# Optimization experiments

Measured on AMD Instinct MI355X. Metric: run time of the kernel, lower is better.

Reference implementation:

```python
import jax, jax.numpy as jnp
import numpy as np

BETA = 0.9      # LIF leak factor
THR = 1.0       # firing threshold
SLOPE = 5.0     # surrogate-gradient sigmoid slope


def spike_fn(v):
    # Heaviside forward, sigmoid surrogate gradient (straight-through).
    hard = (v > THR).astype(v.dtype)
    surr = jax.nn.sigmoid(SLOPE * (v - THR))
    return hard + (surr - jax.lax.stop_gradient(surr))


def setup_inputs() -> dict:
    key = jax.random.key(0)
    ks = jax.random.split(key, 4)
    B, T, IN, H, OUT = 16, 128, 1024, 4096, 1024
    def lin_w(k, out_d, in_d):
        bound = 1.0 / np.sqrt(in_d)
        return jax.random.uniform(k, (out_d, in_d), jnp.float32, -bound, bound)
    return {
        "x": jax.random.normal(ks[0], (B, T, IN), jnp.float32),
        "w1": lin_w(ks[1], H, IN), "b1": jnp.zeros((H,), jnp.float32),
        "w2": lin_w(ks[2], H, H),  "b2": jnp.zeros((H,), jnp.float32),
        "w3": lin_w(ks[3], OUT, H), "b3": jnp.zeros((OUT,), jnp.float32),
    }


def reference(x, w1, b1, w2, b2, w3, b3):
    # x: [B, T, IN]; sequential per-timestep SNN feed-forward, readout = sum over time.
    B = x.shape[0]
    H = w1.shape[0]
    v0 = jnp.zeros((B, H), x.dtype)

    def step(carry, xt):                      # xt: [B, IN]
        v1, v2 = carry
        h1 = xt @ w1.T + b1                   # [B, H]
        v1 = BETA * v1 + h1
        s1 = spike_fn(v1)
        v1 = v1 - s1 * THR                    # soft reset
        h2 = s1 @ w2.T + b2                   # [B, H]
        v2 = BETA * v2 + h2
        s2 = spike_fn(v2)
        v2 = v2 - s2 * THR
        logits = s2 @ w3.T + b3               # [B, OUT]
        return (v1, v2), logits

    _, logits = jax.lax.scan(step, (v0, v0), jnp.swapaxes(x, 0, 1))  # [T, B, OUT]
    return logits.sum(axis=0)                 # readout_mode == 'sum'
```

## Files before the change

### kernel.cpp

```cpp
#include <hip/hip_runtime.h>
#include <hip/hip_bf16.h>

#define B_   16
#define T_   128
#define IN_  1024
#define H_   4096
#define OUT_ 1024
#define M_   (B_ * T_)

typedef __attribute__((ext_vector_type(8))) short short8;
typedef __attribute__((ext_vector_type(4))) float f32x4;
typedef __attribute__((ext_vector_type(4))) int i32x4;
typedef __attribute__((ext_vector_type(4))) unsigned short u16x4;
typedef unsigned short u16;
typedef signed char i8;

__device__ inline u16 f2bf_rne(float f) {
  unsigned u = __float_as_uint(f);
  unsigned r = u + 0x7FFFu + ((u >> 16) & 1u);
  return (u16)(r >> 16);
}
__device__ inline float bf2f(u16 s) {
  return __uint_as_float(((unsigned)s) << 16);
}
__device__ inline int pack4(int a, int b, int c, int d) {
  return (a & 255) | ((b & 255) << 8) | ((c & 255) << 16) | ((d & 255) << 24);
}

__device__ inline void xcd_swizzle(int bid0, int& bnI, int& bmI) {
  const int xcd = bid0 & 7;
  const int loc = bid0 >> 3;
  bnI = (xcd & 3) * 8 + (loc & 7);
  bmI = (xcd >> 2) * 8 + (loc >> 3);
}

#define NX_  (M_ * IN_)
#define NW1_ (H_ * IN_)
#define NW2_ (H_ * H_)

__device__ inline void split4bf(const float4 f, u16* __restrict__ hi,
                                u16* __restrict__ lo, size_t e) {
  u16x4 h, l;
  h.x = f2bf_rne(f.x); l.x = f2bf_rne(f.x - bf2f(h.x));
  h.y = f2bf_rne(f.y); l.y = f2bf_rne(f.y - bf2f(h.y));
  h.z = f2bf_rne(f.z); l.z = f2bf_rne(f.z - bf2f(h.z));
  h.w = f2bf_rne(f.w); l.w = f2bf_rne(f.w - bf2f(h.w));
  *(u16x4*)(hi + e) = h;
  *(u16x4*)(lo + e) = l;
}

__device__ inline void splitw2_1(float w, int& c0, int& c1, int& c2) {
  int wf = __float2int_rn(w * 268435456.0f);
  c0 = (wf + 32768) >> 16;
  int r0 = wf - (c0 << 16);
  if (r0 >= 32640) { c0 += 1; r0 -= 65536; }
  c1 = (r0 + 128) >> 8;
  c2 = r0 - (c1 << 8);
}

__global__ void split_xw1_kernel(const float4* __restrict__ x,
                                 const float4* __restrict__ w1,
                                 u16* __restrict__ xh, u16* __restrict__ xl,
                                 u16* __restrict__ w1h, u16* __restrict__ w1l) {
  const int total4 = (NX_ + NW1_) / 4;
  for (int i = blockIdx.x * blockDim.x + threadIdx.x; i < total4;
       i += gridDim.x * blockDim.x) {
    if (i < NX_ / 4) {
      split4bf(x[i], xh, xl, (size_t)i * 4);
    } else {
      int j = i - NX_ / 4;
      split4bf(w1[j], w1h, w1l, (size_t)j * 4);
    }
  }
}

#define BK1 64

__global__ __launch_bounds__(256, 2) void gemm1_rec(
    const u16* __restrict__ Ah, const u16* __restrict__ Al,
    const u16* __restrict__ Bh, const u16* __restrict__ Bl,
    const float* __restrict__ bias, i8* __restrict__ s1out,
    const float4* __restrict__ w2src,
    i8* __restrict__ p0, i8* __restrict__ p1, i8* __restrict__ p2) {
  __shared__ __align__(16) char smem[65536];
  u16* sAh = (u16*)smem;
  u16* sAl = (u16*)(smem + 16384);
  u16* sBh = (u16*)(smem + 32768);
  u16* sBl = (u16*)(smem + 49152);

  const int tid  = threadIdx.x;
  const int lane = tid & 63;
  const int wid  = tid >> 6;
  const int wm   = (wid >> 1) * 64;
  const int wn   = (wid & 1) * 64;
  const int bid  = blockIdx.y * 32 + blockIdx.x;
  int bnI, bmI;
  xcd_swizzle(bid, bnI, bmI);
  const int bm = bmI * 128;
  const int bn = bnI * 128;

  const int sdst = (tid & 7) * 8;
  const int scol = (((tid & 7) ^ ((tid >> 3) & 7)) * 8);
  const int q8   = (lane >> 4) * 8;
  const int rsw  = (lane & 7) * 8;

  f32x4 acc[4][4];
#pragma unroll
  for (int i = 0; i < 4; ++i)
#pragma unroll
    for (int j = 0; j < 4; ++j) acc[i][j] = (f32x4){0.f, 0.f, 0.f, 0.f};

  const int wbase = bid * 8192 + tid * 2;
  float4 wfa = w2src[wbase];
  float4 wfb = w2src[wbase + 1];

#pragma unroll 1
  for (int it = 0; it < IN_ / BK1; ++it) {
    const int kt = it * BK1;
    __syncthreads();
#pragma unroll
    for (int l = 0; l < 4; ++l) {
      int row = l * 32 + (tid >> 3);
      size_t ga = (size_t)(bm + row) * IN_ + kt + scol;
      size_t gb = (size_t)(bn + row) * IN_ + kt + scol;
      int ld = row * BK1 + sdst;
      __builtin_amdgcn_global_load_lds(
          (const __attribute__((address_space(1))) unsigned int*)(Ah + ga),
          (__attribute__((address_space(3))) unsigned int*)(&sAh[ld]), 16, 0, 0);
      __builtin_amdgcn_global_load_lds(
          (const __attribute__((address_space(1))) unsigned int*)(Al + ga),
          (__attribute__((address_space(3))) unsigned int*)(&sAl[ld]), 16, 0, 0);
      __builtin_amdgcn_global_load_lds(
          (const __attribute__((address_space(1))) unsigned int*)(Bh + gb),
          (__attribute__((address_space(3))) unsigned int*)(&sBh[ld]), 16, 0, 0);
      __builtin_amdgcn_global_load_lds(
          (const __attribute__((address_space(1))) unsigned int*)(Bl + gb),
          (__attribute__((address_space(3))) unsigned int*)(&sBl[ld]), 16, 0, 0);
    }
    __syncthreads();

    const int nit = (it + 1 < 16) ? it + 1 : 15;
    float4 nfa = w2src[wbase + nit * 512];
    float4 nfb = w2src[wbase + nit * 512 + 1];

    {
      const int sbase = bid * 8192 + it * 512 + tid * 2;
#pragma unroll
      for (int u = 0; u < 2; ++u) {
        float4 f = u ? wfb : wfa;
        int a0, a1, a2, b0, b1, b2, c0, c1, c2, d0, d1, d2;
        splitw2_1(f.x, a0, a1, a2);
        splitw2_1(f.y, b0, b1, b2);
        splitw2_1(f.z, c0, c1, c2);
        splitw2_1(f.w, d0, d1, d2);
        size_t e = (size_t)(sbase + u) * 4;
        *(int*)(p0 + e) = pack4(a0, b0, c0, d0);
        *(int*)(p1 + e) = pack4(a1, b1, c1, d1);
        *(int*)(p2 + e) = pack4(a2, b2, c2, d2);
      }
    }

#pragma unroll
    for (int ks = 0; ks < BK1; ks += 32) {
      const int swz = (ks + q8) ^ rsw;
      short8 ah[4], al[4], bh[4], bl[4];
#pragma unroll
      for (int i = 0; i < 4; ++i) {
        int ro = (wm + i * 16 + (lane & 15)) * BK1 + swz;
        ah[i] = *(const short8*)&sAh[ro];
        al[i] = *(const short8*)&sAl[ro];
      }
#pragma unroll
      for (int j = 0; j < 4; ++j) {
        int ro = (wn + j * 16 + (lane & 15)) * BK1 + swz;
        bh[j] = *(const short8*)&sBh[ro];
        bl[j] = *(const short8*)&sBl[ro];
      }
#pragma unroll
      for (int i = 0; i < 4; ++i)
#pragma unroll
        for (int j = 0; j < 4; ++j) {
          acc[i][j] = __builtin_amdgcn_mfma_f32_16x16x32_bf16(ah[i], bh[j], acc[i][j], 0, 0, 0);
          acc[i][j] = __builtin_amdgcn_mfma_f32_16x16x32_bf16(ah[i], bl[j], acc[i][j], 0, 0, 0);
          acc[i][j] = __builtin_amdgcn_mfma_f32_16x16x32_bf16(al[i], bh[j], acc[i][j], 0, 0, 0);
          acc[i][j] = __builtin_amdgcn_mfma_f32_16x16x32_bf16(al[i], bl[j], acc[i][j], 0, 0, 0);
        }
    }

    wfa = nfa;
    wfb = nfb;
  }

  float* hl = (float*)smem;
  const int c = tid & 127;
  const float bv = bias[bn + c];
  float v = 0.0f;
  __syncthreads();
#pragma unroll
  for (int half = 0; half < 2; ++half) {
    if (wm == half * 64) {
#pragma unroll
      for (int i = 0; i < 4; ++i)
#pragma unroll
        for (int j = 0; j < 4; ++j) {
          int col = wn + j * 16 + (lane & 15);
#pragma unroll
          for (int r = 0; r < 4; ++r) {
            int lrow = i * 16 + (lane >> 4) * 4 + r;
            hl[lrow * 128 + col] = acc[i][j][r];
          }
        }
    }
    __syncthreads();
    if (tid < 128) {
      for (int tt = 0; tt < 64; ++tt) {
        float h = hl[tt * 128 + c] + bv;
        v = 0.9f * v + h;
        i8 sp = 0;
        if (v > 1.0f) { sp = 1; v -= 1.0f; }
        s1out[(size_t)(bm + half * 64 + tt) * H_ + bn + c] = sp;
      }
    }
    __syncthreads();
  }
}

#define G2_OFFP1 16384
#define G2_OFFP2 24576
#define G2_OFFP0 32768
#define G2_BUFS  40960

#define G2_GLD(srcp, ldsp)                                                  \
  __builtin_amdgcn_global_load_lds(                                         \
      (const __attribute__((address_space(1))) unsigned int*)(srcp),        \
      (__attribute__((address_space(3))) unsigned int*)(ldsp), 16, 0, 0)

__global__ __launch_bounds__(512, 2) void gemm2_i8(
    const i8* __restrict__ A,
    const i8* __restrict__ P0, const i8* __restrict__ P1,
    const i8* __restrict__ P2,
    const float* __restrict__ bias, float* __restrict__ s2out) {
  __shared__ __align__(16) char smem[81920];

  const int tid  = threadIdx.x;
  const int lane = tid & 63;
  const int wid  = tid >> 6;
  const int wm   = (wid >> 1) * 64;
  const int wn   = (wid & 1) * 64;

  const int bid = blockIdx.x;
  const int xcd = bid & 7, loc = bid >> 3;
  const int bmI = (xcd & 3) * 2 + (loc & 1);
  const int bnI = (xcd >> 2) * 16 + (loc >> 1);
  const int bm = bmI * 256, bn = bnI * 128;

  const int j8   = tid & 7;
  const int r8   = tid >> 3;
  const int cc   = j8 ^ (r8 & 7);
  const int srow = 2 * r8 + (cc >> 2);
  const int scol = (cc & 3) * 16;
  const int dst0 = r8 * 128 + j8 * 16;
  const size_t gA = (size_t)(bm + srow) * H_ + scol;
  const size_t gP = (size_t)(bn + srow) * H_ + scol;

  const int r15 = lane & 15, qk = lane >> 4;
  const int lro = (r15 >> 1) * 128 +
                  (((((r15 & 1) << 2) + qk) ^ ((r15 >> 1) & 7)) * 16);
  const int abase = wm * 64 + lro;
  const int bbase = wn * 64 + lro;

  i32x4 acc0[4][4], acc1[4][4], acc2[4][4];
#pragma unroll
  for (int i = 0; i < 4; ++i)
#pragma unroll
    for (int j = 0; j < 4; ++j) {
      acc0[i][j] = (i32x4){0, 0, 0, 0};
      acc1[i][j] = (i32x4){0, 0, 0, 0};
      acc2[i][j] = (i32x4){0, 0, 0, 0};
    }

  G2_GLD(A + gA, smem + dst0);
  G2_GLD(A + gA + (size_t)128 * H_, smem + 8192 + dst0);
  G2_GLD(P1 + gP, smem + G2_OFFP1 + dst0);
  G2_GLD(P2 + gP, smem + G2_OFFP2 + dst0);
  G2_GLD(P0 + gP, smem + G2_OFFP0 + dst0);
  G2_GLD(A + gA + 64, smem + G2_BUFS + dst0);
  G2_GLD(A + gA + (size_t)128 * H_ + 64, smem + G2_BUFS + 8192 + dst0);
  G2_GLD(P1 + gP + 64, smem + G2_BUFS + G2_OFFP1 + dst0);
  asm volatile("s_waitcnt vmcnt(5)" ::: "memory");
  __builtin_amdgcn_s_barrier();

#pragma unroll 1
  for (int t = 0; t < 64; ++t) {
    char* cur = smem + (t & 1) * G2_BUFS;
    char* nxt = smem + ((t + 1) & 1) * G2_BUFS;
    const int kt1 = (t < 63 ? t + 1 : 63) << 6;
    const int kt2 = (t < 62 ? t + 2 : 63) << 6;

    i32x4 a[4], b[4];

#pragma unroll
    for (int i = 0; i < 4; ++i)
      a[i] = *(const i32x4*)(cur + abase + i * 1024);
#pragma unroll
    for (int j = 0; j < 4; ++j)
      b[j] = *(const i32x4*)(cur + G2_OFFP1 + bbase + j * 1024);
    G2_GLD(P2 + gP + kt1, nxt + G2_OFFP2 + dst0);
    G2_GLD(P0 + gP + kt1, nxt + G2_OFFP0 + dst0);
    __builtin_amdgcn_s_barrier();
    asm volatile("s_waitcnt lgkmcnt(0)" ::: "memory");
    __builtin_amdgcn_s_setprio(1);
#pragma unroll
    for (int i = 0; i < 4; ++i)
#pragma unroll
      for (int j = 0; j < 4; ++j)
        acc1[i][j] = __builtin_amdgcn_mfma_i32_16x16x64_i8(a[i], b[j], acc1[i][j], 0, 0, 0);
    __builtin_amdgcn_s_setprio(0);
    asm volatile("s_waitcnt vmcnt(5)" ::: "memory");
    __builtin_amdgcn_s_barrier();

#pragma unroll
    for (int j = 0; j < 4; ++j)
      b[j] = *(const i32x4*)(cur + G2_OFFP2 + bbase + j * 1024);
    G2_GLD(A + gA + kt2, cur + dst0);
    G2_GLD(A + gA + (size_t)128 * H_ + kt2, cur + 8192 + dst0);
    G2_GLD(P1 + gP + kt2, cur + G2_OFFP1 + dst0);
    __builtin_amdgcn_s_barrier();
    asm volatile("s_waitcnt lgkmcnt(0)" ::: "memory");
    __builtin_amdgcn_s_setprio(1);
#pragma unroll
    for (int i = 0; i < 4; ++i)
#pragma unroll
      for (int j = 0; j < 4; ++j)
        acc2[i][j] = __builtin_amdgcn_mfma_i32_16x16x64_i8(a[i], b[j], acc2[i][j], 0, 0, 0);
    __builtin_amdgcn_s_setprio(0);
    __builtin_amdgcn_s_barrier();

#pragma unroll
    for (int j = 0; j < 4; ++j)
      b[j] = *(const i32x4*)(cur + G2_OFFP0 + bbase + j * 1024);
    __builtin_amdgcn_s_barrier();
    asm volatile("s_waitcnt lgkmcnt(0)" ::: "memory");
    __builtin_amdgcn_s_setprio(1);
#pragma unroll
    for (int i = 0; i < 4; ++i)
#pragma unroll
      for (int j = 0; j < 4; ++j)
        acc0[i][j] = __builtin_amdgcn_mfma_i32_16x16x64_i8(a[i], b[j], acc0[i][j], 0, 0, 0);
    __builtin_amdgcn_s_setprio(0);
    asm volatile("s_waitcnt vmcnt(5)" ::: "memory");
    __builtin_amdgcn_s_barrier();
  }

  float* hl = (float*)smem;
  const int ec = tid & 127;
  const float bv = bias[bn + ec];
  asm volatile("s_waitcnt vmcnt(0)" ::: "memory");
  __syncthreads();
#pragma unroll
  for (int hb = 0; hb < 2; ++hb) {
    float v = 0.0f, cnt = 0.0f;
#pragma unroll
    for (int half = 0; half < 2; ++half) {
      const int hq = hb * 2 + half;
      if (wm == hq * 64) {
#pragma unroll
        for (int i = 0; i < 4; ++i)
#pragma unroll
          for (int j = 0; j < 4; ++j) {
            int col = wn + j * 16 + (lane & 15);
#pragma unroll
            for (int r = 0; r < 4; ++r) {
              int lrow = i * 16 + (lane >> 4) * 4 + r;
              float val = 0x1p-28f * (float)((acc1[i][j][r] << 8) + acc2[i][j][r]) +
                          0x1p-12f * (float)acc0[i][j][r];
              hl[lrow * 128 + col] = val;
            }
          }
      }
      __syncthreads();
      if (tid < 128) {
        for (int tt = 0; tt < 64; ++tt) {
          float h = hl[tt * 128 + ec] + bv;
          v = 0.9f * v + h;
          if (v > 1.0f) { cnt += 1.0f; v -= 1.0f; }
        }
      }
      __syncthreads();
    }
    if (tid < 128) s2out[(size_t)(2 * bmI + hb) * H_ + bn + ec] = cnt;
  }
}

__global__ void out_gemm_kernel(const float* __restrict__ s2sum,
                                const float* __restrict__ w3,
                                const float* __restrict__ b3,
                                float* __restrict__ out) {
  int o = blockIdx.x;
  int lane = threadIdx.x;
  float acc[B_];
#pragma unroll
  for (int b = 0; b < B_; ++b) acc[b] = 0.f;
  const float* wrow = w3 + (size_t)o * H_;
  for (int i = 0; i < H_ / 64; ++i) {
    float w = wrow[i * 64 + lane];
#pragma unroll
    for (int b = 0; b < B_; ++b)
      acc[b] += w * s2sum[b * H_ + i * 64 + lane];
  }
#pragma unroll
  for (int b = 0; b < B_; ++b) {
    float v = acc[b];
#pragma unroll
    for (int off = 32; off > 0; off >>= 1) v += __shfl_xor(v, off);
    if (lane == b) out[b * OUT_ + o] = v + (float)T_ * b3[o];
  }
}

extern "C" void kernel_launch(void* const* d_in, const int* in_sizes, int n_in,
                              void* d_out, int out_size, void* d_ws, size_t ws_size,
                              hipStream_t stream) {
  const float* x  = (const float*)d_in[0];
  const float* w1 = (const float*)d_in[1];
  const float* b1 = (const float*)d_in[2];
  const float* w2 = (const float*)d_in[3];
  const float* b2 = (const float*)d_in[4];
  const float* w3 = (const float*)d_in[5];
  const float* b3 = (const float*)d_in[6];
  float* out = (float*)d_out;

  char* ws = (char*)d_ws;
  i8*    s1    = (i8*)(ws);
  u16*   x_hi  = (u16*)(ws + 8388608);
  u16*   x_lo  = (u16*)(ws + 12582912);
  u16*   w1_hi = (u16*)(ws + 16777216);
  u16*   w1_lo = (u16*)(ws + 25165824);
  i8*    w2p0  = (i8*)(ws + 33554432);
  i8*    w2p1  = (i8*)(ws + 50331648);
  i8*    w2p2  = (i8*)(ws + 67108864);
  float* s2sum = (float*)(ws + 83886080);

  split_xw1_kernel<<<1024, 256, 0, stream>>>((const float4*)x, (const float4*)w1,
                                             x_hi, x_lo, w1_hi, w1_lo);

  dim3 g1(H_ / 128, M_ / 128);
  gemm1_rec<<<g1, 256, 0, stream>>>(x_hi, x_lo, w1_hi, w1_lo, b1, s1,
                                    (const float4*)w2, w2p0, w2p1, w2p2);

  gemm2_i8<<<dim3(256), 512, 0, stream>>>(s1, w2p0, w2p1, w2p2, b2, s2sum);

  out_gemm_kernel<<<OUT_, 64, 0, stream>>>(s2sum, w3, b3, out);
}
```

Before: 174.8 us.

## Software-pipeline LDS fragment loads against MFMAs in int8 gemm2 main loop

Restructures the gemm2 K loop so each LDS fragment load for the next MFMA group is issued before the current MFMA group, using register double-buffered A/B1 fragments and a loop unrolled by two over the two shared-memory buffers. Barrier and vmcnt waits are reshuffled (fewer barriers per tile, vmcnt 3/2 instead of 5), and sched_barriers pin the ordering. The goal is to hide LDS read latency and cut the waits between the three accumulation phases. In exchange it uses more registers, which may hurt at launch bounds of 512 threads with 2 blocks, and the relaxed waits carry a risk of races.

```diff
diff --git a/kernel.cpp b/kernel.cpp
--- a/kernel.cpp
+++ b/kernel.cpp
@@ -235,6 +235,62 @@
       (const __attribute__((address_space(1))) unsigned int*)(srcp),        \
       (__attribute__((address_space(3))) unsigned int*)(ldsp), 16, 0, 0)
 
+#define G2_FENCE asm volatile("" ::: "memory")
+
+__device__ __forceinline__ void g2_ld4(i32x4 (&f)[4], const char* base) {
+#pragma unroll
+  for (int j = 0; j < 4; ++j) f[j] = *(const i32x4*)(base + j * 1024);
+}
+
+__device__ __forceinline__ void g2_mfma16(const i32x4 (&a)[4], const i32x4 (&b)[4],
+                                          i32x4 (&acc)[4][4]) {
+#pragma unroll
+  for (int i = 0; i < 4; ++i)
+#pragma unroll
+    for (int j = 0; j < 4; ++j)
+      acc[i][j] = __builtin_amdgcn_mfma_i32_16x16x64_i8(a[i], b[j], acc[i][j], 0, 0, 0);
+}
+
+#define G2_TILE(T, CUR, NXT, FAI, FB1I, FAO, FB1O)                           \
+  {                                                                          \
+    const int kt1 = ((T) < 63 ? (T) + 1 : 63) << 6;                          \
+    const int kt2 = ((T) < 62 ? (T) + 2 : 63) << 6;                          \
+                                                  \
+    asm volatile("s_waitcnt vmcnt(3)" ::: "memory");       \
+    __builtin_amdgcn_s_barrier();                                            \
+    G2_FENCE;                                                                \
+    g2_ld4(fB2, (CUR) + G2_OFFP2 + bbase);                                   \
+    G2_GLD(P2 + gP + kt1, (NXT) + G2_OFFP2 + dst0);                          \
+    G2_GLD(P0 + gP + kt1, (NXT) + G2_OFFP0 + dst0);                          \
+    G2_FENCE;                                                                \
+    __builtin_amdgcn_sched_barrier(0);                                       \
+    __builtin_amdgcn_s_setprio(1);                                           \
+    g2_mfma16(FAI, FB1I, acc1);                                              \
+    __builtin_amdgcn_s_setprio(0);                                           \
+                                                  \
+    asm volatile("s_waitcnt vmcnt(2)" ::: "memory");     \
+    __builtin_amdgcn_s_barrier();                                            \
+    G2_FENCE;                                                                \
+    g2_ld4(fB0, (CUR) + G2_OFFP0 + bbase);                                   \
+    G2_GLD(A + gA + kt2, (CUR) + dst0);                                      \
+    G2_GLD(A + gA + (size_t)128 * H_ + kt2, (CUR) + 8192 + dst0);            \
+    G2_GLD(P1 + gP + kt2, (CUR) + G2_OFFP1 + dst0);                          \
+    G2_FENCE;                                                                \
+    __builtin_amdgcn_sched_barrier(0);                                       \
+    __builtin_amdgcn_s_setprio(1);                                           \
+    g2_mfma16(FAI, fB2, acc2);                                               \
+    __builtin_amdgcn_s_setprio(0);                                           \
+            \
+    G2_FENCE;                                                                \
+    g2_ld4(FAO, (NXT) + abase);                                              \
+    g2_ld4(FB1O, (NXT) + G2_OFFP1 + bbase);                                  \
+    G2_FENCE;                                                                \
+    __builtin_amdgcn_sched_barrier(0);                                       \
+    __builtin_amdgcn_s_setprio(1);                                           \
+    g2_mfma16(FAI, fB0, acc0);                                               \
+    __builtin_amdgcn_s_setprio(0);                                           \
+  }
+
 __global__ __launch_bounds__(512, 2) void gemm2_i8(
     const i8* __restrict__ A,
     const i8* __restrict__ P0, const i8* __restrict__ P1,
@@ -279,77 +335,28 @@
       acc2[i][j] = (i32x4){0, 0, 0, 0};
     }
 
-  G2_GLD(A + gA, smem + dst0);
-  G2_GLD(A + gA + (size_t)128 * H_, smem + 8192 + dst0);
-  G2_GLD(P1 + gP, smem + G2_OFFP1 + dst0);
-  G2_GLD(P2 + gP, smem + G2_OFFP2 + dst0);
-  G2_GLD(P0 + gP, smem + G2_OFFP0 + dst0);
-  G2_GLD(A + gA + 64, smem + G2_BUFS + dst0);
-  G2_GLD(A + gA + (size_t)128 * H_ + 64, smem + G2_BUFS + 8192 + dst0);
-  G2_GLD(P1 + gP + 64, smem + G2_BUFS + G2_OFFP1 + dst0);
+  i32x4 fAa[4], fB1a[4], fAb[4], fB1b[4], fB2[4], fB0[4];
+  char* const buf0 = smem;
+  char* const buf1 = smem + G2_BUFS;
+
+  G2_GLD(A + gA, buf0 + dst0);
+  G2_GLD(A + gA + (size_t)128 * H_, buf0 + 8192 + dst0);
+  G2_GLD(P1 + gP, buf0 + G2_OFFP1 + dst0);
+  G2_GLD(P2 + gP, buf0 + G2_OFFP2 + dst0);
+  G2_GLD(P0 + gP, buf0 + G2_OFFP0 + dst0);
+  G2_GLD(A + gA + 64, buf1 + dst0);
+  G2_GLD(A + gA + (size_t)128 * H_ + 64, buf1 + 8192 + dst0);
+  G2_GLD(P1 + gP + 64, buf1 + G2_OFFP1 + dst0);
   asm volatile("s_waitcnt vmcnt(5)" ::: "memory");
   __builtin_amdgcn_s_barrier();
+  G2_FENCE;
+  g2_ld4(fAa, buf0 + abase);
+  g2_ld4(fB1a, buf0 + G2_OFFP1 + bbase);
 
 #pragma unroll 1
-  for (int t = 0; t < 64; ++t) {
-    char* cur = smem + (t & 1) * G2_BUFS;
-    char* nxt = smem + ((t + 1) & 1) * G2_BUFS;
-    const int kt1 = (t < 63 ? t + 1 : 63) << 6;
-    const int kt2 = (t < 62 ? t + 2 : 63) << 6;
-
-    i32x4 a[4], b[4];
-
-#pragma unroll
-    for (int i = 0; i < 4; ++i)
-      a[i] = *(const i32x4*)(cur + abase + i * 1024);
-#pragma unroll
-    for (int j = 0; j < 4; ++j)
-      b[j] = *(const i32x4*)(cur + G2_OFFP1 + bbase + j * 1024);
-    G2_GLD(P2 + gP + kt1, nxt + G2_OFFP2 + dst0);
-    G2_GLD(P0 + gP + kt1, nxt + G2_OFFP0 + dst0);
-    __builtin_amdgcn_s_barrier();
-    asm volatile("s_waitcnt lgkmcnt(0)" ::: "memory");
-    __builtin_amdgcn_s_setprio(1);
-#pragma unroll
-    for (int i = 0; i < 4; ++i)
-#pragma unroll
-      for (int j = 0; j < 4; ++j)
-        acc1[i][j] = __builtin_amdgcn_mfma_i32_16x16x64_i8(a[i], b[j], acc1[i][j], 0, 0, 0);
-    __builtin_amdgcn_s_setprio(0);
-    asm volatile("s_waitcnt vmcnt(5)" ::: "memory");
-    __builtin_amdgcn_s_barrier();
-
-#pragma unroll
-    for (int j = 0; j < 4; ++j)
-      b[j] = *(const i32x4*)(cur + G2_OFFP2 + bbase + j * 1024);
-    G2_GLD(A + gA + kt2, cur + dst0);
-    G2_GLD(A + gA + (size_t)128 * H_ + kt2, cur + 8192 + dst0);
-    G2_GLD(P1 + gP + kt2, cur + G2_OFFP1 + dst0);
-    __builtin_amdgcn_s_barrier();
-    asm volatile("s_waitcnt lgkmcnt(0)" ::: "memory");
-    __builtin_amdgcn_s_setprio(1);
-#pragma unroll
-    for (int i = 0; i < 4; ++i)
-#pragma unroll
-      for (int j = 0; j < 4; ++j)
-        acc2[i][j] = __builtin_amdgcn_mfma_i32_16x16x64_i8(a[i], b[j], acc2[i][j], 0, 0, 0);
-    __builtin_amdgcn_s_setprio(0);
-    __builtin_amdgcn_s_barrier();
-
-#pragma unroll
-    for (int j = 0; j < 4; ++j)
-      b[j] = *(const i32x4*)(cur + G2_OFFP0 + bbase + j * 1024);
-    __builtin_amdgcn_s_barrier();
-    asm volatile("s_waitcnt lgkmcnt(0)" ::: "memory");
-    __builtin_amdgcn_s_setprio(1);
-#pragma unroll
-    for (int i = 0; i < 4; ++i)
-#pragma unroll
-      for (int j = 0; j < 4; ++j)
-        acc0[i][j] = __builtin_amdgcn_mfma_i32_16x16x64_i8(a[i], b[j], acc0[i][j], 0, 0, 0);
-    __builtin_amdgcn_s_setprio(0);
-    asm volatile("s_waitcnt vmcnt(5)" ::: "memory");
-    __builtin_amdgcn_s_barrier();
+  for (int t = 0; t < 64; t += 2) {
+    G2_TILE(t,     buf0, buf1, fAa, fB1a, fAb, fB1b);
+    G2_TILE(t + 1, buf1, buf0, fAb, fB1b, fAa, fB1a);
   }
 
   float* hl = (float*)smem;
```

New measurement: 283.9 us. 1.62x slower.

## Split int8 gemm2 into two K-passes with smaller 128x128 tiles

Applied to the files above, without the earlier changes.

The int8 three-plane gemm2 drops its 256x128 tile with 512 threads and a triple-buffered interleaved schedule. It now uses 128x128 tiles with 256 threads over a 32x16 grid, which cuts LDS to 48KB and allows more blocks to reside at once. The K loop runs twice: the first pass accumulates the P1 and P2 planes into float, the second accumulates the P0 plane, each with simple double buffering. This lowers register pressure and LDS use, but the A tile (s1) is loaded from global memory twice and each block covers half as many rows, so A reuse per B load drops.

```diff
diff --git a/kernel.cpp b/kernel.cpp
--- a/kernel.cpp
+++ b/kernel.cpp
@@ -225,34 +225,40 @@
   }
 }
 
-#define G2_OFFP1 16384
-#define G2_OFFP2 24576
-#define G2_OFFP0 32768
-#define G2_BUFS  40960
+#define G2A_BUFS 24576
+#define G2B_BUFS 16384
 
 #define G2_GLD(srcp, ldsp)                                                  \
   __builtin_amdgcn_global_load_lds(                                         \
       (const __attribute__((address_space(1))) unsigned int*)(srcp),        \
       (__attribute__((address_space(3))) unsigned int*)(ldsp), 16, 0, 0)
 
-__global__ __launch_bounds__(512, 2) void gemm2_i8(
+__device__ __forceinline__ void g2_mfma16(const i32x4 (&a)[4], const i32x4 (&b)[4],
+                                          i32x4 (&acc)[4][4]) {
+#pragma unroll
+  for (int i = 0; i < 4; ++i)
+#pragma unroll
+    for (int j = 0; j < 4; ++j)
+      acc[i][j] = __builtin_amdgcn_mfma_i32_16x16x64_i8(a[i], b[j], acc[i][j], 0, 0, 0);
+}
+
+__global__ __launch_bounds__(256, 2) void gemm2_i8(
     const i8* __restrict__ A,
     const i8* __restrict__ P0, const i8* __restrict__ P1,
     const i8* __restrict__ P2,
     const float* __restrict__ bias, float* __restrict__ s2out) {
-  __shared__ __align__(16) char smem[81920];
+  __shared__ __align__(16) char smem[49152];
 
   const int tid  = threadIdx.x;
   const int lane = tid & 63;
   const int wid  = tid >> 6;
   const int wm   = (wid >> 1) * 64;
   const int wn   = (wid & 1) * 64;
-
-  const int bid = blockIdx.x;
-  const int xcd = bid & 7, loc = bid >> 3;
-  const int bmI = (xcd & 3) * 2 + (loc & 1);
-  const int bnI = (xcd >> 2) * 16 + (loc >> 1);
-  const int bm = bmI * 256, bn = bnI * 128;
+  const int bid  = blockIdx.y * 32 + blockIdx.x;
+  int bnI, bmI;
+  xcd_swizzle(bid, bnI, bmI);
+  const int bm = bmI * 128;
+  const int bn = bnI * 128;
 
   const int j8   = tid & 7;
   const int r8   = tid >> 3;
@@ -260,8 +266,10 @@
   const int srow = 2 * r8 + (cc >> 2);
   const int scol = (cc & 3) * 16;
   const int dst0 = r8 * 128 + j8 * 16;
-  const size_t gA = (size_t)(bm + srow) * H_ + scol;
-  const size_t gP = (size_t)(bn + srow) * H_ + scol;
+  const size_t gA0 = (size_t)(bm + srow) * H_ + scol;
+  const size_t gA1 = gA0 + (size_t)64 * H_;
+  const size_t gB0 = (size_t)(bn + srow) * H_ + scol;
+  const size_t gB1 = gB0 + (size_t)64 * H_;
 
   const int r15 = lane & 15, qk = lane >> 4;
   const int lro = (r15 >> 1) * 128 +
@@ -269,127 +277,135 @@
   const int abase = wm * 64 + lro;
   const int bbase = wn * 64 + lro;
 
-  i32x4 acc0[4][4], acc1[4][4], acc2[4][4];
-#pragma unroll
-  for (int i = 0; i < 4; ++i)
-#pragma unroll
-    for (int j = 0; j < 4; ++j) {
-      acc0[i][j] = (i32x4){0, 0, 0, 0};
-      acc1[i][j] = (i32x4){0, 0, 0, 0};
-      acc2[i][j] = (i32x4){0, 0, 0, 0};
-    }
-
-  G2_GLD(A + gA, smem + dst0);
-  G2_GLD(A + gA + (size_t)128 * H_, smem + 8192 + dst0);
-  G2_GLD(P1 + gP, smem + G2_OFFP1 + dst0);
-  G2_GLD(P2 + gP, smem + G2_OFFP2 + dst0);
-  G2_GLD(P0 + gP, smem + G2_OFFP0 + dst0);
-  G2_GLD(A + gA + 64, smem + G2_BUFS + dst0);
-  G2_GLD(A + gA + (size_t)128 * H_ + 64, smem + G2_BUFS + 8192 + dst0);
-  G2_GLD(P1 + gP + 64, smem + G2_BUFS + G2_OFFP1 + dst0);
-  asm volatile("s_waitcnt vmcnt(5)" ::: "memory");
+  f32x4 facc[4][4];
+
+  {
+    i32x4 acc1[4][4], acc2[4][4];
+#pragma unroll
+    for (int i = 0; i < 4; ++i)
+#pragma unroll
+      for (int j = 0; j < 4; ++j) {
+        acc1[i][j] = (i32x4){0, 0, 0, 0};
+        acc2[i][j] = (i32x4){0, 0, 0, 0};
+      }
+
+#define LA_STAGE(KT, BUF)                                   \
+    G2_GLD(A + gA0 + (KT), (BUF) + dst0);                   \
+    G2_GLD(A + gA1 + (KT), (BUF) + 4096 + dst0);            \
+    G2_GLD(P1 + gB0 + (KT), (BUF) + 8192 + dst0);           \
+    G2_GLD(P1 + gB1 + (KT), (BUF) + 12288 + dst0);          \
+    G2_GLD(P2 + gB0 + (KT), (BUF) + 16384 + dst0);          \
+    G2_GLD(P2 + gB1 + (KT), (BUF) + 20480 + dst0);
+
+    LA_STAGE(0, smem)
+
+#pragma unroll 1
+    for (int t = 0; t < 64; ++t) {
+      char* cur = smem + (t & 1) * G2A_BUFS;
+      char* nxt = smem + ((t + 1) & 1) * G2A_BUFS;
+      const int ktn = (t < 63 ? t + 1 : 63) * 64;
+      LA_STAGE(ktn, nxt)
+      asm volatile("s_waitcnt vmcnt(6)" ::: "memory");
+      __builtin_amdgcn_s_barrier();
+      i32x4 a[4], b1[4], b2[4];
+#pragma unroll
+      for (int i = 0; i < 4; ++i)
+        a[i] = *(const i32x4*)(cur + abase + i * 1024);
+#pragma unroll
+      for (int j = 0; j < 4; ++j) {
+        b1[j] = *(const i32x4*)(cur + 8192 + bbase + j * 1024);
+        b2[j] = *(const i32x4*)(cur + 16384 + bbase + j * 1024);
+      }
+      __builtin_amdgcn_s_setprio(1);
+      g2_mfma16(a, b1, acc1);
+      g2_mfma16(a, b2, acc2);
+      __builtin_amdgcn_s_setprio(0);
+      __builtin_amdgcn_s_barrier();
+    }
+#undef LA_STAGE
+
+#pragma unroll
+    for (int i = 0; i < 4; ++i)
+#pragma unroll
+      for (int j = 0; j < 4; ++j)
+#pragma unroll
+        for (int r = 0; r < 4; ++r)
+          facc[i][j][r] = 0x1p-28f * (float)((acc1[i][j][r] << 8) + acc2[i][j][r]);
+  }
+
+  asm volatile("s_waitcnt vmcnt(0)" ::: "memory");
   __builtin_amdgcn_s_barrier();
 
+  i32x4 acc0[4][4];
+  {
+#pragma unroll
+    for (int i = 0; i < 4; ++i)
+#pragma unroll
+      for (int j = 0; j < 4; ++j) acc0[i][j] = (i32x4){0, 0, 0, 0};
+
+#define LB_STAGE(KT, BUF)                                   \
+    G2_GLD(A + gA0 + (KT), (BUF) + dst0);                   \
+    G2_GLD(A + gA1 + (KT), (BUF) + 4096 + dst0);            \
+    G2_GLD(P0 + gB0 + (KT), (BUF) + 8192 + dst0);           \
+    G2_GLD(P0 + gB1 + (KT), (BUF) + 12288 + dst0);
+
+    LB_STAGE(0, smem)
+
 #pragma unroll 1
-  for (int t = 0; t < 64; ++t) {
-    char* cur = smem + (t & 1) * G2_BUFS;
-    char* nxt = smem + ((t + 1) & 1) * G2_BUFS;
-    const int kt1 = (t < 63 ? t + 1 : 63) << 6;
-    const int kt2 = (t < 62 ? t + 2 : 63) << 6;
-
-    i32x4 a[4], b[4];
-
-#pragma unroll
-    for (int i = 0; i < 4; ++i)
-      a[i] = *(const i32x4*)(cur + abase + i * 1024);
-#pragma unroll
-    for (int j = 0; j < 4; ++j)
-      b[j] = *(const i32x4*)(cur + G2_OFFP1 + bbase + j * 1024);
-    G2_GLD(P2 + gP + kt1, nxt + G2_OFFP2 + dst0);
-    G2_GLD(P0 + gP + kt1, nxt + G2_OFFP0 + dst0);
-    __builtin_amdgcn_s_barrier();
-    asm volatile("s_waitcnt lgkmcnt(0)" ::: "memory");
-    __builtin_amdgcn_s_setprio(1);
-#pragma unroll
-    for (int i = 0; i < 4; ++i)
+    for (int t = 0; t < 64; ++t) {
+      char* cur = smem + (t & 1) * G2B_BUFS;
+      char* nxt = smem + ((t + 1) & 1) * G2B_BUFS;
+      const int ktn = (t < 63 ? t + 1 : 63) * 64;
+      LB_STAGE(ktn, nxt)
+      asm volatile("s_waitcnt vmcnt(4)" ::: "memory");
+      __builtin_amdgcn_s_barrier();
+      i32x4 a[4], b[4];
+#pragma unroll
+      for (int i = 0; i < 4; ++i)
+        a[i] = *(const i32x4*)(cur + abase + i * 1024);
 #pragma unroll
       for (int j = 0; j < 4; ++j)
-        acc1[i][j] = __builtin_amdgcn_mfma_i32_16x16x64_i8(a[i], b[j], acc1[i][j], 0, 0, 0);
-    __builtin_amdgcn_s_setprio(0);
-    asm volatile("s_waitcnt vmcnt(5)" ::: "memory");
-    __builtin_amdgcn_s_barrier();
-
-#pragma unroll
-    for (int j = 0; j < 4; ++j)
-      b[j] = *(const i32x4*)(cur + G2_OFFP2 + bbase + j * 1024);
-    G2_GLD(A + gA + kt2, cur + dst0);
-    G2_GLD(A + gA + (size_t)128 * H_ + kt2, cur + 8192 + dst0);
-    G2_GLD(P1 + gP + kt2, cur + G2_OFFP1 + dst0);
-    __builtin_amdgcn_s_barrier();
-    asm volatile("s_waitcnt lgkmcnt(0)" ::: "memory");
-    __builtin_amdgcn_s_setprio(1);
-#pragma unroll
-    for (int i = 0; i < 4; ++i)
-#pragma unroll
-      for (int j = 0; j < 4; ++j)
-        acc2[i][j] = __builtin_amdgcn_mfma_i32_16x16x64_i8(a[i], b[j], acc2[i][j], 0, 0, 0);
-    __builtin_amdgcn_s_setprio(0);
-    __builtin_amdgcn_s_barrier();
-
-#pragma unroll
-    for (int j = 0; j < 4; ++j)
-      b[j] = *(const i32x4*)(cur + G2_OFFP0 + bbase + j * 1024);
-    __builtin_amdgcn_s_barrier();
-    asm volatile("s_waitcnt lgkmcnt(0)" ::: "memory");
-    __builtin_amdgcn_s_setprio(1);
-#pragma unroll
-    for (int i = 0; i < 4; ++i)
-#pragma unroll
-      for (int j = 0; j < 4; ++j)
-        acc0[i][j] = __builtin_amdgcn_mfma_i32_16x16x64_i8(a[i], b[j], acc0[i][j], 0, 0, 0);
-    __builtin_amdgcn_s_setprio(0);
-    asm volatile("s_waitcnt vmcnt(5)" ::: "memory");
-    __builtin_amdgcn_s_barrier();
+        b[j] = *(const i32x4*)(cur + 8192 + bbase + j * 1024);
+      __builtin_amdgcn_s_setprio(1);
+      g2_mfma16(a, b, acc0);
+      __builtin_amdgcn_s_setprio(0);
+      __builtin_amdgcn_s_barrier();
+    }
+#undef LB_STAGE
   }
 
   float* hl = (float*)smem;
-  const int ec = tid & 127;
-  const float bv = bias[bn + ec];
+  const int c = tid & 127;
+  const float bv = bias[bn + c];
+  float v = 0.0f, cnt = 0.0f;
   asm volatile("s_waitcnt vmcnt(0)" ::: "memory");
   __syncthreads();
 #pragma unroll
-  for (int hb = 0; hb < 2; ++hb) {
-    float v = 0.0f, cnt = 0.0f;
-#pragma unroll
-    for (int half = 0; half < 2; ++half) {
-      const int hq = hb * 2 + half;
-      if (wm == hq * 64) {
-#pragma unroll
-        for (int i = 0; i < 4; ++i)
-#pragma unroll
-          for (int j = 0; j < 4; ++j) {
-            int col = wn + j * 16 + (lane & 15);
-#pragma unroll
-            for (int r = 0; r < 4; ++r) {
-              int lrow = i * 16 + (lane >> 4) * 4 + r;
-              float val = 0x1p-28f * (float)((acc1[i][j][r] << 8) + acc2[i][j][r]) +
-                          0x1p-12f * (float)acc0[i][j][r];
-              hl[lrow * 128 + col] = val;
-            }
+  for (int half = 0; half < 2; ++half) {
+    if (wm == half * 64) {
+#pragma unroll
+      for (int i = 0; i < 4; ++i)
+#pragma unroll
+        for (int j = 0; j < 4; ++j) {
+          int col = wn + j * 16 + (lane & 15);
+#pragma unroll
+          for (int r = 0; r < 4; ++r) {
+            int lrow = i * 16 + (lane >> 4) * 4 + r;
+            hl[lrow * 128 + col] = facc[i][j][r] + 0x1p-12f * (float)acc0[i][j][r];
           }
-      }
-      __syncthreads();
-      if (tid < 128) {
-        for (int tt = 0; tt < 64; ++tt) {
-          float h = hl[tt * 128 + ec] + bv;
-          v = 0.9f * v + h;
-          if (v > 1.0f) { cnt += 1.0f; v -= 1.0f; }
         }
-      }
-      __syncthreads();
-    }
-    if (tid < 128) s2out[(size_t)(2 * bmI + hb) * H_ + bn + ec] = cnt;
-  }
+    }
+    __syncthreads();
+    if (tid < 128) {
+      for (int tt = 0; tt < 64; ++tt) {
+        float h = hl[tt * 128 + c] + bv;
+        v = 0.9f * v + h;
+        if (v > 1.0f) { cnt += 1.0f; v -= 1.0f; }
+      }
+    }
+    __syncthreads();
+  }
+  if (tid < 128) s2out[(size_t)bmI * H_ + bn + c] = cnt;
 }
 
 __global__ void out_gemm_kernel(const float* __restrict__ s2sum,
@@ -447,7 +463,7 @@
   gemm1_rec<<<g1, 256, 0, stream>>>(x_hi, x_lo, w1_hi, w1_lo, b1, s1,
                                     (const float4*)w2, w2p0, w2p1, w2p2);
 
-  gemm2_i8<<<dim3(256), 512, 0, stream>>>(s1, w2p0, w2p1, w2p2, b2, s2sum);
+  gemm2_i8<<<g1, 256, 0, stream>>>(s1, w2p0, w2p1, w2p2, b2, s2sum);
 
   out_gemm_kernel<<<OUT_, 64, 0, stream>>>(s2sum, w3, b3, out);
 }
```

Result: slower. 193.0 us (+10.4%).
